# Kernel tuning notes

Measured on AMD Instinct MI355X. Metric: run time of the kernel, lower is better.

Reference implementation:

```python
import jax, jax.numpy as jnp
import numpy as np

B, S, N, E = 4, 256, 257, 256  # batch, seq_len, num_nodes (=S+1), num_edges (=S)
IN, OUT, EDIM = 128, 128, 16


def setup_inputs() -> dict:
    key = jax.random.key(0)
    k = jax.random.split(key, 7)
    x = jax.random.normal(k[0], (B, S, N, IN), jnp.float32)
    ei = jax.random.randint(k[1], (B, S, E, 2), 0, N)
    drop = jax.random.uniform(k[2], (B, S, E, 2)) < 0.05
    edge_index = jnp.where(drop, -1, ei)
    edge_attr = jax.random.normal(k[3], (B, S, E, EDIM), jnp.float32)
    node_mask = jnp.ones((B, S, N), dtype=bool)  # accepted but unused by forward
    edge_mask = jax.random.uniform(k[4], (B, S, E)) > 0.1
    W = jax.random.normal(k[5], (IN, OUT), jnp.float32) * (1.0 / np.sqrt(IN))
    a = jax.random.normal(k[6], (2 * OUT + EDIM, 1), jnp.float32) * 0.05
    return {"x": x, "edge_index": edge_index, "edge_attr": edge_attr,
            "node_mask": node_mask, "edge_mask": edge_mask, "W": W, "a": a}


def reference(x, edge_index, edge_attr, node_mask, edge_mask, W, a):
    # x: [B,S,N,IN] -> h: [B,S,N,D]
    h = x @ W
    Bq, Sq = h.shape[0], h.shape[1]
    src_idx = edge_index[..., 0]  # [B,S,E]
    tgt_idx = edge_index[..., 1]

    def gather(idx):  # [B,S,E] -> [B,S,E,D], gather node features along node dim
        return jnp.take_along_axis(h, jnp.clip(idx, 0, None)[..., None], axis=2)

    # src/tgt features, zeroed where index < 0 (invalid edge endpoint)
    src = jnp.where((src_idx >= 0)[..., None], gather(src_idx), 0.0)
    tgt = jnp.where((tgt_idx >= 0)[..., None], gather(tgt_idx), 0.0)

    # attention logits over concatenated [src | tgt | edge_attr]
    cat = jnp.concatenate([src, tgt, edge_attr], axis=-1)  # [B,S,E,2D+edim]
    e = jax.nn.leaky_relu((cat @ a)[..., 0], negative_slope=0.2)  # [B,S,E]
    e = jnp.where(edge_mask, e, -jnp.inf)
    # rows with no finite entry are zeroed (-> uniform softmax), as in torch code
    all_invalid = ~jnp.isfinite(e).any(axis=-1, keepdims=True)
    e = jnp.where(all_invalid, 0.0, e)
    alpha = jax.nn.softmax(e, axis=-1)  # [B,S,E]

    # masked edges get index 0 (they still contribute alpha-weighted feats to node 0,
    # matching the original scatter semantics)
    vsrc = jnp.where(edge_mask, src_idx, 0)
    vtgt = jnp.where(edge_mask, tgt_idx, 0)
    x_src = jnp.take_along_axis(h, vsrc[..., None], axis=2) * alpha[..., None]
    x_tgt = jnp.take_along_axis(h, vtgt[..., None], axis=2) * alpha[..., None]

    # scatter-add over edges into node buffer (equivalent to the torch 5D
    # scatter_ + sum over the edge dim, without materializing [B,S,E,N,D])
    bi = jnp.arange(Bq)[:, None, None]
    si = jnp.arange(Sq)[None, :, None]
    agg = (jnp.zeros(h.shape, h.dtype)
           .at[bi, si, vtgt].add(x_src)
           .at[bi, si, vsrc].add(x_tgt))
    return jax.nn.elu(agg)
```

## Files before the change

kernel.cpp:

```cpp
#include <hip/hip_runtime.h>
#include <cfloat>
#include <cmath>


#define BB 4
#define SS 256
#define NNODE 257
#define EE 256
#define DIN 128
#define DOUT 128
#define EDIMC 16
#define NMASK (BB * SS * EE)
#define MROWS (BB * SS * NNODE)

#define WS_FLAG_OFF  0
#define WS_MASK_OFF  1024
#define WS_ALPHA_OFF 266240
#define WS_PQ_OFF    (WS_ALPHA_OFF + NMASK * 4)
#define WS_PT_OFF    (WS_PQ_OFF + MROWS * 4)
#define WS_NEEDED    (WS_PT_OFF + MROWS * 4)

__global__ void detect_mask_kernel(const unsigned int* __restrict__ m, int* flag) {
    unsigned int v = 0;
    for (int i = threadIdx.x; i < 256; i += 64) v |= m[i];
    int bad = (v > 1u) ? 1 : 0;
    bad = __any(bad) ? 1 : 0;
    if (threadIdx.x == 0) *flag = bad;
}

__global__ __launch_bounds__(256) void mask_canon_kernel(
        const int* __restrict__ m32, const unsigned char* __restrict__ m8,
        const int* __restrict__ flag, unsigned char* __restrict__ out) {
    const bool byteLayout = (*flag != 0);
    int i = blockIdx.x * 256 + threadIdx.x;
    if (i < NMASK) out[i] = byteLayout ? (m8[i] != 0) : (m32[i] != 0);
}

__global__ __launch_bounds__(256) void gemm_kernel(const float* __restrict__ x,
                                                   const float* __restrict__ W,
                                                   const float* __restrict__ a,
                                                   float* __restrict__ h,
                                                   float* __restrict__ pq,
                                                   float* __restrict__ pt) {
    __shared__ float xs[32][132];
    __shared__ float wsh[32][132];
    const int tid = threadIdx.x;
    const long m0 = (long)blockIdx.x * 128;
    const int tm = tid >> 4;
    const int tn = tid & 15;
    const int mr = tm * 8, nr = tn * 8;
    float acc[8][8];
#pragma unroll
    for (int i = 0; i < 8; ++i)
#pragma unroll
        for (int j = 0; j < 8; ++j) acc[i][j] = 0.f;

    for (int kt = 0; kt < 4; ++kt) {
#pragma unroll
        for (int j = 0; j < 4; ++j) {
            int idx = j * 256 + tid;
            int row = idx >> 3;
            int kq  = idx & 7;
            float4 v = *reinterpret_cast<const float4*>(
                x + (m0 + row) * DIN + kt * 32 + kq * 4);
            xs[kq * 4 + 0][row] = v.x;
            xs[kq * 4 + 1][row] = v.y;
            xs[kq * 4 + 2][row] = v.z;
            xs[kq * 4 + 3][row] = v.w;
        }
#pragma unroll
        for (int j = 0; j < 4; ++j) {
            int idx = j * 256 + tid;
            int row = idx >> 5;
            int nq  = idx & 31;
            float4 v = *reinterpret_cast<const float4*>(
                W + (kt * 32 + row) * DOUT + nq * 4);
            *reinterpret_cast<float4*>(&wsh[row][nq * 4]) = v;
        }
        __syncthreads();
#pragma unroll
        for (int k = 0; k < 32; ++k) {
            float4 a0 = *reinterpret_cast<const float4*>(&xs[k][mr]);
            float4 a1 = *reinterpret_cast<const float4*>(&xs[k][mr + 4]);
            float4 b0 = *reinterpret_cast<const float4*>(&wsh[k][nr]);
            float4 b1 = *reinterpret_cast<const float4*>(&wsh[k][nr + 4]);
            float av[8] = {a0.x, a0.y, a0.z, a0.w, a1.x, a1.y, a1.z, a1.w};
            float bv[8] = {b0.x, b0.y, b0.z, b0.w, b1.x, b1.y, b1.z, b1.w};
#pragma unroll
            for (int i = 0; i < 8; ++i)
#pragma unroll
                for (int jj = 0; jj < 8; ++jj)
                    acc[i][jj] = fmaf(av[i], bv[jj], acc[i][jj]);
        }
        __syncthreads();
    }
#pragma unroll
    for (int i = 0; i < 8; ++i) {
        float* dst = h + (m0 + mr + i) * DOUT + nr;
        *reinterpret_cast<float4*>(dst) =
            make_float4(acc[i][0], acc[i][1], acc[i][2], acc[i][3]);
        *reinterpret_cast<float4*>(dst + 4) =
            make_float4(acc[i][4], acc[i][5], acc[i][6], acc[i][7]);
    }

    if (pq != nullptr) {
        float aq[8], at_[8];
#pragma unroll
        for (int j = 0; j < 8; ++j) {
            aq[j]  = a[nr + j];
            at_[j] = a[DOUT + nr + j];
        }
#pragma unroll
        for (int i = 0; i < 8; ++i) {
            float s = 0.f, t = 0.f;
#pragma unroll
            for (int j = 0; j < 8; ++j) {
                s = fmaf(acc[i][j], aq[j], s);
                t = fmaf(acc[i][j], at_[j], t);
            }
#pragma unroll
            for (int o = 1; o < 16; o <<= 1) {
                s += __shfl_xor(s, o);
                t += __shfl_xor(t, o);
            }
            if (tn == 0) {
                pq[m0 + mr + i] = s;
                pt[m0 + mr + i] = t;
            }
        }
    }
}

__global__ __launch_bounds__(256) void alpha2_kernel(
        const float* __restrict__ pq, const float* __restrict__ pt,
        const int* __restrict__ eidx, const float* __restrict__ eattr,
        const unsigned char* __restrict__ emask, const float* __restrict__ a,
        float* __restrict__ alpha_out) {
    __shared__ float ae[EDIMC];
    __shared__ float red[4];
    __shared__ int redi[4];
    const int tid = threadIdx.x;
    const int bs = blockIdx.x;
    const int lane = tid & 63, wave = tid >> 6;
    if (tid < EDIMC) ae[tid] = a[2 * DOUT + tid];
    __syncthreads();

    const long ebase = (long)bs * EE + tid;
    const int si = eidx[2 * ebase];
    const int ti = eidx[2 * ebase + 1];
    const float4* ea4 = reinterpret_cast<const float4*>(eattr + ebase * EDIMC);
    float dea = 0.f;
#pragma unroll
    for (int j = 0; j < 4; ++j) {
        float4 u = ea4[j];
        dea += u.x * ae[4 * j] + u.y * ae[4 * j + 1] +
               u.z * ae[4 * j + 2] + u.w * ae[4 * j + 3];
    }
    const long nb = (long)bs * NNODE;
    float val = (si >= 0 ? pq[nb + si] : 0.f) + (ti >= 0 ? pt[nb + ti] : 0.f) + dea;
    val = val > 0.f ? val : 0.2f * val;
    const bool m = emask[ebase] != 0;

    float lg = m ? val : -FLT_MAX;
    float wm = lg;
    int anyv = m ? 1 : 0;
#pragma unroll
    for (int o = 32; o > 0; o >>= 1) {
        wm = fmaxf(wm, __shfl_xor(wm, o));
        anyv |= __shfl_xor(anyv, o);
    }
    if (lane == 0) { red[wave] = wm; redi[wave] = anyv; }
    __syncthreads();
    const float gmax = fmaxf(fmaxf(red[0], red[1]), fmaxf(red[2], red[3]));
    const int ganyv = redi[0] | redi[1] | redi[2] | redi[3];
    float ex = m ? expf(val - gmax) : 0.f;
    float sm = ex;
#pragma unroll
    for (int o = 32; o > 0; o >>= 1) sm += __shfl_xor(sm, o);
    __syncthreads();
    if (lane == 0) red[wave] = sm;
    __syncthreads();
    const float gsum = red[0] + red[1] + red[2] + red[3];
    alpha_out[ebase] = ganyv ? ex / gsum : (1.0f / EE);
}

__global__ __launch_bounds__(256) void alpha_kernel(
        const float* __restrict__ h, const int* __restrict__ eidx,
        const float* __restrict__ eattr, const unsigned char* __restrict__ emask,
        const float* __restrict__ a, float* __restrict__ alpha_out) {
    __shared__ float pq[NNODE], pt[NNODE];
    __shared__ float ae[EDIMC];
    __shared__ float red[4];
    __shared__ int redi[4];
    const int tid = threadIdx.x;
    const int bs = blockIdx.x;
    const int lane = tid & 63, wave = tid >> 6;
    if (tid < EDIMC) ae[tid] = a[2 * DOUT + tid];
    const float a0 = a[lane], a1 = a[lane + 64];
    const float a2 = a[128 + lane], a3 = a[192 + lane];
    const float* hb = h + (long)bs * NNODE * DIN;
    for (int n = wave; n < NNODE; n += 4) {
        const float* hr = hb + n * DIN;
        float v0 = hr[lane], v1 = hr[lane + 64];
        float s = v0 * a0 + v1 * a1;
        float t = v0 * a2 + v1 * a3;
#pragma unroll
        for (int o = 32; o > 0; o >>= 1) {
            s += __shfl_xor(s, o);
            t += __shfl_xor(t, o);
        }
        if (lane == 0) { pq[n] = s; pt[n] = t; }
    }
    __syncthreads();

    const long ebase = (long)bs * EE + tid;
    const int si = eidx[2 * ebase];
    const int ti = eidx[2 * ebase + 1];
    const float4* ea4 = reinterpret_cast<const float4*>(eattr + ebase * EDIMC);
    float dea = 0.f;
#pragma unroll
    for (int j = 0; j < 4; ++j) {
        float4 u = ea4[j];
        dea += u.x * ae[4 * j] + u.y * ae[4 * j + 1] +
               u.z * ae[4 * j + 2] + u.w * ae[4 * j + 3];
    }
    float val = (si >= 0 ? pq[si] : 0.f) + (ti >= 0 ? pt[ti] : 0.f) + dea;
    val = val > 0.f ? val : 0.2f * val;
    const bool m = emask[ebase] != 0;

    float lg = m ? val : -FLT_MAX;
    float wm = lg;
    int anyv = m ? 1 : 0;
#pragma unroll
    for (int o = 32; o > 0; o >>= 1) {
        wm = fmaxf(wm, __shfl_xor(wm, o));
        anyv |= __shfl_xor(anyv, o);
    }
    if (lane == 0) { red[wave] = wm; redi[wave] = anyv; }
    __syncthreads();
    const float gmax = fmaxf(fmaxf(red[0], red[1]), fmaxf(red[2], red[3]));
    const int ganyv = redi[0] | redi[1] | redi[2] | redi[3];
    float ex = m ? expf(val - gmax) : 0.f;
    float sm = ex;
#pragma unroll
    for (int o = 32; o > 0; o >>= 1) sm += __shfl_xor(sm, o);
    __syncthreads();
    if (lane == 0) red[wave] = sm;
    __syncthreads();
    const float gsum = red[0] + red[1] + red[2] + red[3];
    alpha_out[ebase] = ganyv ? ex / gsum : (1.0f / EE);
}

#define DSL 16
#define PAD 17
__global__ __launch_bounds__(256) void agg_kernel(
        const float* __restrict__ h, const int* __restrict__ eidx,
        const unsigned char* __restrict__ emask, const float* __restrict__ alpha,
        float* __restrict__ out) {
    __shared__ float hs[NNODE * PAD];
    __shared__ float acc[NNODE * PAD];
    __shared__ float meta_a[EE];
    __shared__ int   meta_v[EE];
    const int tid = threadIdx.x;
    const int bs = blockIdx.x;
    const int dbase = blockIdx.y * DSL;
    const int slot = tid >> 4, d = tid & 15;

    const float* hb = h + (long)bs * NNODE * DIN + dbase;

    for (int i = tid; i < NNODE * 4; i += 256) {
        int row = i >> 2, q = i & 3;
        float4 v = *reinterpret_cast<const float4*>(hb + (long)row * DIN + q * 4);
        float* dst = &hs[row * PAD + q * 4];
        dst[0] = v.x; dst[1] = v.y; dst[2] = v.z; dst[3] = v.w;
    }
    for (int i = tid; i < NNODE * PAD; i += 256) acc[i] = 0.f;
    {
        const long eb = (long)bs * EE + tid;
        const int si = eidx[2 * eb];
        const int ti = eidx[2 * eb + 1];
        const bool m = emask[eb] != 0;
        int vs = m ? si : 0; if (vs < 0) vs += NNODE;
        int vt = m ? ti : 0; if (vt < 0) vt += NNODE;
        meta_a[tid] = alpha[eb];
        meta_v[tid] = vs | (vt << 16);
    }
    __syncthreads();

#pragma unroll 4
    for (int e0 = 0; e0 < EE; e0 += 16) {
        const int e = e0 + slot;
        const float al = meta_a[e];
        if (al != 0.f) {
            const int pv = meta_v[e];
            const int vs = pv & 0xffff, vt = pv >> 16;
            const float hsv = hs[vs * PAD + d];
            const float htv = hs[vt * PAD + d];
            atomicAdd(&acc[vt * PAD + d], al * hsv);
            atomicAdd(&acc[vs * PAD + d], al * htv);
        }
    }
    __syncthreads();

    float* ob = out + (long)bs * NNODE * DIN + dbase;
    for (int n = slot; n < NNODE; n += 16) {
        const float v = acc[n * PAD + d];
        ob[(long)n * DIN + d] = v > 0.f ? v : expm1f(v);
    }
}

extern "C" void kernel_launch(void* const* d_in, const int* in_sizes, int n_in,
                              void* d_out, int out_size, void* d_ws, size_t ws_size,
                              hipStream_t stream) {
    const float* x     = (const float*)d_in[0];
    const int* eidx    = (const int*)d_in[1];
    const float* eattr = (const float*)d_in[2];
    const void* emraw  = d_in[4];
    const float* W     = (const float*)d_in[5];
    const float* a     = (const float*)d_in[6];
    float* out = (float*)d_out;

    char* ws = (char*)d_ws;
    int* flag            = (int*)(ws + WS_FLAG_OFF);
    unsigned char* mask8 = (unsigned char*)(ws + WS_MASK_OFF);
    float* alpha         = (float*)(ws + WS_ALPHA_OFF);
    float* h             = out;
    const bool fused     = (ws_size >= (size_t)WS_NEEDED);
    float* pq            = fused ? (float*)(ws + WS_PQ_OFF) : nullptr;
    float* pt            = fused ? (float*)(ws + WS_PT_OFF) : nullptr;

    detect_mask_kernel<<<1, 64, 0, stream>>>((const unsigned int*)emraw, flag);
    mask_canon_kernel<<<NMASK / 256, 256, 0, stream>>>(
        (const int*)emraw, (const unsigned char*)emraw, flag, mask8);

    const int M_BLOCKS = MROWS / 128;
    gemm_kernel<<<M_BLOCKS, 256, 0, stream>>>(x, W, a, h, pq, pt);
    if (fused) {
        alpha2_kernel<<<BB * SS, 256, 0, stream>>>(pq, pt, eidx, eattr, mask8, a, alpha);
    } else {
        alpha_kernel<<<BB * SS, 256, 0, stream>>>(h, eidx, eattr, mask8, a, alpha);
    }
    agg_kernel<<<dim3(BB * SS, 8), 256, 0, stream>>>(h, eidx, mask8, alpha, out);
}
```

Baseline: 626.9 us.

## Use split-bf16 MFMA GEMM for projection and widen aggregation blocks

Replaces the FP32 SIMT GEMM with a matrix-core kernel that splits x and W into high and low bf16 parts and accumulates three MFMA products, which keeps close to FP32 accuracy. A small prep kernel writes W transposed as bf16 hi/lo into the workspace. The attention projections pq/pt are now reduced through shared-memory atomics. Separately, the aggregation kernel moves to 512 threads so 32 edges are processed per iteration. The GEMM rewrite targets compute time in the large projection, at the cost of three MFMAs per tile, extra conversion work, and a larger workspace requirement.

```diff
diff --git a/kernel.cpp b/kernel.cpp
--- a/kernel.cpp
+++ b/kernel.cpp
@@ -18,7 +18,21 @@
 #define WS_ALPHA_OFF 266240
 #define WS_PQ_OFF    (WS_ALPHA_OFF + NMASK * 4)
 #define WS_PT_OFF    (WS_PQ_OFF + MROWS * 4)
-#define WS_NEEDED    (WS_PT_OFF + MROWS * 4)
+#define WS_WTHI_OFF  (WS_PT_OFF + MROWS * 4)
+#define WS_WTLO_OFF  (WS_WTHI_OFF + DIN * DOUT * 2)
+#define WS_NEEDED    (WS_WTLO_OFF + DIN * DOUT * 2)
+
+typedef __attribute__((ext_vector_type(8))) short bf16x8;
+typedef __attribute__((ext_vector_type(4))) float f32x4;
+
+__device__ __forceinline__ unsigned short f2bf(float f) {
+    unsigned u = __float_as_uint(f);
+    u += 0x7fff + ((u >> 16) & 1);
+    return (unsigned short)(u >> 16);
+}
+__device__ __forceinline__ float bf2f(unsigned short h) {
+    return __uint_as_float((unsigned)h << 16);
+}
 
 __global__ void detect_mask_kernel(const unsigned int* __restrict__ m, int* flag) {
     unsigned int v = 0;
@@ -36,43 +50,185 @@
     if (i < NMASK) out[i] = byteLayout ? (m8[i] != 0) : (m32[i] != 0);
 }
 
+__global__ __launch_bounds__(256) void wprep_kernel(
+        const float* __restrict__ W, unsigned short* __restrict__ wthi,
+        unsigned short* __restrict__ wtlo) {
+    const int tid = threadIdx.x;
+    for (int i = tid; i < DIN * DOUT; i += 256) {
+        const int k = i >> 7, n = i & 127;
+        const float w = W[i];
+        const unsigned short hi = f2bf(w);
+        const unsigned short lo = f2bf(w - bf2f(hi));
+        wthi[n * DIN + k] = hi;
+        wtlo[n * DIN + k] = lo;
+    }
+}
+
+#define XPAD 40
+__global__ __launch_bounds__(256) void mfma_gemm_kernel(
+        const float* __restrict__ x, const unsigned short* __restrict__ wthi,
+        const unsigned short* __restrict__ wtlo, const float* __restrict__ a,
+        float* __restrict__ h, float* __restrict__ pq, float* __restrict__ pt) {
+    __shared__ unsigned short xhi[128][XPAD];
+    __shared__ unsigned short xlo[128][XPAD];
+    __shared__ unsigned short bhi[128][XPAD];
+    __shared__ unsigned short blo[128][XPAD];
+    __shared__ float pqs[128], pts[128];
+
+    const int tid = threadIdx.x;
+    const long m0 = (long)blockIdx.x * 128;
+    const int wave = tid >> 6, lane = tid & 63;
+    const int wm = wave >> 1, wn = wave & 1;
+    const int lrow = lane & 15;
+    const int lk8 = (lane >> 4) * 8;
+
+    if (tid < 128) { pqs[tid] = 0.f; pts[tid] = 0.f; }
+
+    f32x4 acc[4][4];
+#pragma unroll
+    for (int i = 0; i < 4; ++i)
+#pragma unroll
+        for (int j = 0; j < 4; ++j) acc[i][j] = (f32x4){0.f, 0.f, 0.f, 0.f};
+
+    const int srow = tid >> 1;
+    const int sk = (tid & 1) * 16;
+
+    for (int kt = 0; kt < 4; ++kt) {
+        __syncthreads();
+        {
+            const float* src = x + (m0 + srow) * DIN + kt * 32 + sk;
+#pragma unroll
+            for (int q = 0; q < 4; ++q) {
+                float4 v = *reinterpret_cast<const float4*>(src + q * 4);
+                ushort4 hi, lo;
+                hi.x = f2bf(v.x); lo.x = f2bf(v.x - bf2f(hi.x));
+                hi.y = f2bf(v.y); lo.y = f2bf(v.y - bf2f(hi.y));
+                hi.z = f2bf(v.z); lo.z = f2bf(v.z - bf2f(hi.z));
+                hi.w = f2bf(v.w); lo.w = f2bf(v.w - bf2f(hi.w));
+                *reinterpret_cast<ushort4*>(&xhi[srow][sk + q * 4]) = hi;
+                *reinterpret_cast<ushort4*>(&xlo[srow][sk + q * 4]) = lo;
+            }
+        }
+        {
+            const int n = tid >> 1;
+            const int kh = (tid & 1) * 16;
+            const unsigned short* sh = wthi + n * DIN + kt * 32 + kh;
+            const unsigned short* sl = wtlo + n * DIN + kt * 32 + kh;
+            *reinterpret_cast<uint4*>(&bhi[n][kh]) =
+                *reinterpret_cast<const uint4*>(sh);
+            *reinterpret_cast<uint4*>(&bhi[n][kh + 8]) =
+                *reinterpret_cast<const uint4*>(sh + 8);
+            *reinterpret_cast<uint4*>(&blo[n][kh]) =
+                *reinterpret_cast<const uint4*>(sl);
+            *reinterpret_cast<uint4*>(&blo[n][kh + 8]) =
+                *reinterpret_cast<const uint4*>(sl + 8);
+        }
+        __syncthreads();
+
+        bf16x8 Bh[4], Bl[4];
+#pragma unroll
+        for (int fn = 0; fn < 4; ++fn) {
+            const int n = wn * 64 + fn * 16 + lrow;
+            Bh[fn] = *reinterpret_cast<const bf16x8*>(&bhi[n][lk8]);
+            Bl[fn] = *reinterpret_cast<const bf16x8*>(&blo[n][lk8]);
+        }
+#pragma unroll
+        for (int fm = 0; fm < 4; ++fm) {
+            const int r = wm * 64 + fm * 16 + lrow;
+            bf16x8 Ah = *reinterpret_cast<const bf16x8*>(&xhi[r][lk8]);
+            bf16x8 Al = *reinterpret_cast<const bf16x8*>(&xlo[r][lk8]);
+#pragma unroll
+            for (int fn = 0; fn < 4; ++fn)
+                acc[fm][fn] = __builtin_amdgcn_mfma_f32_16x16x32_bf16(
+                    Ah, Bh[fn], acc[fm][fn], 0, 0, 0);
+#pragma unroll
+            for (int fn = 0; fn < 4; ++fn)
+                acc[fm][fn] = __builtin_amdgcn_mfma_f32_16x16x32_bf16(
+                    Ah, Bl[fn], acc[fm][fn], 0, 0, 0);
+#pragma unroll
+            for (int fn = 0; fn < 4; ++fn)
+                acc[fm][fn] = __builtin_amdgcn_mfma_f32_16x16x32_bf16(
+                    Al, Bh[fn], acc[fm][fn], 0, 0, 0);
+        }
+    }
+
+    const int qrow = (lane >> 4) * 4;
+    const int ccol = lane & 15;
+#pragma unroll
+    for (int fm = 0; fm < 4; ++fm) {
+#pragma unroll
+        for (int fn = 0; fn < 4; ++fn) {
+            float* dst = h + (m0 + wm * 64 + fm * 16 + qrow) * DOUT +
+                         wn * 64 + fn * 16 + ccol;
+#pragma unroll
+            for (int r = 0; r < 4; ++r) dst[(long)r * DOUT] = acc[fm][fn][r];
+        }
+    }
+
+    if (pq != nullptr) {
+        float aq[4], at_[4];
+#pragma unroll
+        for (int fn = 0; fn < 4; ++fn) {
+            aq[fn]  = a[wn * 64 + fn * 16 + ccol];
+            at_[fn] = a[DOUT + wn * 64 + fn * 16 + ccol];
+        }
+#pragma unroll
+        for (int fm = 0; fm < 4; ++fm) {
+#pragma unroll
+            for (int r = 0; r < 4; ++r) {
+                float s = 0.f, t = 0.f;
+#pragma unroll
+                for (int fn = 0; fn < 4; ++fn) {
+                    s = fmaf(acc[fm][fn][r], aq[fn], s);
+                    t = fmaf(acc[fm][fn][r], at_[fn], t);
+                }
+#pragma unroll
+                for (int o = 1; o < 16; o <<= 1) {
+                    s += __shfl_xor(s, o);
+                    t += __shfl_xor(t, o);
+                }
+                if (ccol == 0) {
+                    atomicAdd(&pqs[wm * 64 + fm * 16 + qrow + r], s);
+                    atomicAdd(&pts[wm * 64 + fm * 16 + qrow + r], t);
+                }
+            }
+        }
+        __syncthreads();
+        if (tid < 128) {
+            pq[m0 + tid] = pqs[tid];
+            pt[m0 + tid] = pts[tid];
+        }
+    }
+}
+
 __global__ __launch_bounds__(256) void gemm_kernel(const float* __restrict__ x,
                                                    const float* __restrict__ W,
-                                                   const float* __restrict__ a,
-                                                   float* __restrict__ h,
-                                                   float* __restrict__ pq,
-                                                   float* __restrict__ pt) {
+                                                   float* __restrict__ h) {
     __shared__ float xs[32][132];
     __shared__ float wsh[32][132];
     const int tid = threadIdx.x;
     const long m0 = (long)blockIdx.x * 128;
-    const int tm = tid >> 4;
-    const int tn = tid & 15;
+    const int tm = tid >> 4, tn = tid & 15;
     const int mr = tm * 8, nr = tn * 8;
     float acc[8][8];
 #pragma unroll
     for (int i = 0; i < 8; ++i)
 #pragma unroll
         for (int j = 0; j < 8; ++j) acc[i][j] = 0.f;
-
     for (int kt = 0; kt < 4; ++kt) {
 #pragma unroll
         for (int j = 0; j < 4; ++j) {
             int idx = j * 256 + tid;
-            int row = idx >> 3;
-            int kq  = idx & 7;
+            int row = idx >> 3, kq = idx & 7;
             float4 v = *reinterpret_cast<const float4*>(
                 x + (m0 + row) * DIN + kt * 32 + kq * 4);
-            xs[kq * 4 + 0][row] = v.x;
-            xs[kq * 4 + 1][row] = v.y;
-            xs[kq * 4 + 2][row] = v.z;
-            xs[kq * 4 + 3][row] = v.w;
+            xs[kq * 4 + 0][row] = v.x; xs[kq * 4 + 1][row] = v.y;
+            xs[kq * 4 + 2][row] = v.z; xs[kq * 4 + 3][row] = v.w;
         }
 #pragma unroll
         for (int j = 0; j < 4; ++j) {
             int idx = j * 256 + tid;
-            int row = idx >> 5;
-            int nq  = idx & 31;
+            int row = idx >> 5, nq = idx & 31;
             float4 v = *reinterpret_cast<const float4*>(
                 W + (kt * 32 + row) * DOUT + nq * 4);
             *reinterpret_cast<float4*>(&wsh[row][nq * 4]) = v;
@@ -101,33 +257,6 @@
             make_float4(acc[i][0], acc[i][1], acc[i][2], acc[i][3]);
         *reinterpret_cast<float4*>(dst + 4) =
             make_float4(acc[i][4], acc[i][5], acc[i][6], acc[i][7]);
-    }
-
-    if (pq != nullptr) {
-        float aq[8], at_[8];
-#pragma unroll
-        for (int j = 0; j < 8; ++j) {
-            aq[j]  = a[nr + j];
-            at_[j] = a[DOUT + nr + j];
-        }
-#pragma unroll
-        for (int i = 0; i < 8; ++i) {
-            float s = 0.f, t = 0.f;
-#pragma unroll
-            for (int j = 0; j < 8; ++j) {
-                s = fmaf(acc[i][j], aq[j], s);
-                t = fmaf(acc[i][j], at_[j], t);
-            }
-#pragma unroll
-            for (int o = 1; o < 16; o <<= 1) {
-                s += __shfl_xor(s, o);
-                t += __shfl_xor(t, o);
-            }
-            if (tn == 0) {
-                pq[m0 + mr + i] = s;
-                pt[m0 + mr + i] = t;
-            }
-        }
     }
 }
 
@@ -161,8 +290,7 @@
     val = val > 0.f ? val : 0.2f * val;
     const bool m = emask[ebase] != 0;
 
-    float lg = m ? val : -FLT_MAX;
-    float wm = lg;
+    float wm = m ? val : -FLT_MAX;
     int anyv = m ? 1 : 0;
 #pragma unroll
     for (int o = 32; o > 0; o >>= 1) {
@@ -228,8 +356,7 @@
     val = val > 0.f ? val : 0.2f * val;
     const bool m = emask[ebase] != 0;
 
-    float lg = m ? val : -FLT_MAX;
-    float wm = lg;
+    float wm = m ? val : -FLT_MAX;
     int anyv = m ? 1 : 0;
 #pragma unroll
     for (int o = 32; o > 0; o >>= 1) {
@@ -253,7 +380,7 @@
 
 #define DSL 16
 #define PAD 17
-__global__ __launch_bounds__(256) void agg_kernel(
+__global__ __launch_bounds__(512) void agg_kernel(
         const float* __restrict__ h, const int* __restrict__ eidx,
         const unsigned char* __restrict__ emask, const float* __restrict__ alpha,
         float* __restrict__ out) {
@@ -268,14 +395,14 @@
 
     const float* hb = h + (long)bs * NNODE * DIN + dbase;
 
-    for (int i = tid; i < NNODE * 4; i += 256) {
+    for (int i = tid; i < NNODE * 4; i += 512) {
         int row = i >> 2, q = i & 3;
         float4 v = *reinterpret_cast<const float4*>(hb + (long)row * DIN + q * 4);
         float* dst = &hs[row * PAD + q * 4];
         dst[0] = v.x; dst[1] = v.y; dst[2] = v.z; dst[3] = v.w;
     }
-    for (int i = tid; i < NNODE * PAD; i += 256) acc[i] = 0.f;
-    {
+    for (int i = tid; i < NNODE * PAD; i += 512) acc[i] = 0.f;
+    if (tid < EE) {
         const long eb = (long)bs * EE + tid;
         const int si = eidx[2 * eb];
         const int ti = eidx[2 * eb + 1];
@@ -288,7 +415,7 @@
     __syncthreads();
 
 #pragma unroll 4
-    for (int e0 = 0; e0 < EE; e0 += 16) {
+    for (int e0 = 0; e0 < EE; e0 += 32) {
         const int e = e0 + slot;
         const float al = meta_a[e];
         if (al != 0.f) {
@@ -303,7 +430,7 @@
     __syncthreads();
 
     float* ob = out + (long)bs * NNODE * DIN + dbase;
-    for (int n = slot; n < NNODE; n += 16) {
+    for (int n = slot; n < NNODE; n += 32) {
         const float v = acc[n * PAD + d];
         ob[(long)n * DIN + d] = v > 0.f ? v : expm1f(v);
     }
@@ -328,17 +455,21 @@
     const bool fused     = (ws_size >= (size_t)WS_NEEDED);
     float* pq            = fused ? (float*)(ws + WS_PQ_OFF) : nullptr;
     float* pt            = fused ? (float*)(ws + WS_PT_OFF) : nullptr;
+    unsigned short* wthi = (unsigned short*)(ws + WS_WTHI_OFF);
+    unsigned short* wtlo = (unsigned short*)(ws + WS_WTLO_OFF);
 
     detect_mask_kernel<<<1, 64, 0, stream>>>((const unsigned int*)emraw, flag);
     mask_canon_kernel<<<NMASK / 256, 256, 0, stream>>>(
         (const int*)emraw, (const unsigned char*)emraw, flag, mask8);
 
     const int M_BLOCKS = MROWS / 128;
-    gemm_kernel<<<M_BLOCKS, 256, 0, stream>>>(x, W, a, h, pq, pt);
     if (fused) {
+        wprep_kernel<<<1, 256, 0, stream>>>(W, wthi, wtlo);
+        mfma_gemm_kernel<<<M_BLOCKS, 256, 0, stream>>>(x, wthi, wtlo, a, h, pq, pt);
         alpha2_kernel<<<BB * SS, 256, 0, stream>>>(pq, pt, eidx, eattr, mask8, a, alpha);
     } else {
+        gemm_kernel<<<M_BLOCKS, 256, 0, stream>>>(x, W, h);
         alpha_kernel<<<BB * SS, 256, 0, stream>>>(h, eidx, eattr, mask8, a, alpha);
     }
-    agg_kernel<<<dim3(BB * SS, 8), 256, 0, stream>>>(h, eidx, mask8, alpha, out);
-}
+    agg_kernel<<<dim3(BB * SS, 8), 512, 0, stream>>>(h, eidx, mask8, alpha, out);
+}
```

Result: slower. 642.6 us (+2.5%).

## Fuse projection, attention and aggregation per graph using linearity of W

Applied to the files above, without the earlier changes.

Because the scatter-add is linear, the kernel aggregates raw x rows weighted by alpha first and multiplies by W afterwards, all in one per-(b,s) block. Attention logits come from x·(W a) vectors precomputed in a tiny prep kernel, so the full h matrix is never materialised. The final 257x128x128 product uses bf16 MFMA with hi/lo splitting (three products) to keep near-fp32 accuracy. This removes the large h write and reread and two kernel launches. In exchange it adds shared-memory atomics on a large LDS buffer, which limits occupancy, and a small accuracy change from the split-bf16 arithmetic.

```diff
diff --git a/kernel.cpp b/kernel.cpp
--- a/kernel.cpp
+++ b/kernel.cpp
@@ -15,10 +15,24 @@
 
 #define WS_FLAG_OFF  0
 #define WS_MASK_OFF  1024
-#define WS_ALPHA_OFF 266240
-#define WS_PQ_OFF    (WS_ALPHA_OFF + NMASK * 4)
-#define WS_PT_OFF    (WS_PQ_OFF + MROWS * 4)
-#define WS_NEEDED    (WS_PT_OFF + MROWS * 4)
+#define WS_WTHI_OFF  266240
+#define WS_WTLO_OFF  (WS_WTHI_OFF + 32768)
+#define WS_WAQ_OFF   (WS_WTLO_OFF + 32768)
+#define WS_WAT_OFF   (WS_WAQ_OFF + 512)
+#define WS_ALPHA_OFF (WS_WAT_OFF + 512)
+#define WS_NEEDED    (WS_ALPHA_OFF + NMASK * 4)
+
+typedef __attribute__((ext_vector_type(8))) short bf16x8;
+typedef __attribute__((ext_vector_type(4))) float f32x4;
+
+__device__ __forceinline__ unsigned short f2bf(float f) {
+    unsigned u = __float_as_uint(f);
+    u += 0x7fff + ((u >> 16) & 1);
+    return (unsigned short)(u >> 16);
+}
+__device__ __forceinline__ float bf2f(unsigned short h) {
+    return __uint_as_float((unsigned)h << 16);
+}
 
 __global__ void detect_mask_kernel(const unsigned int* __restrict__ m, int* flag) {
     unsigned int v = 0;
@@ -36,43 +50,249 @@
     if (i < NMASK) out[i] = byteLayout ? (m8[i] != 0) : (m32[i] != 0);
 }
 
+__global__ __launch_bounds__(256) void wprep_kernel(
+        const float* __restrict__ W, const float* __restrict__ a,
+        unsigned short* __restrict__ wthi, unsigned short* __restrict__ wtlo,
+        float* __restrict__ waq, float* __restrict__ wat) {
+    const int tid = threadIdx.x;
+    for (int i = tid; i < DIN * DOUT; i += 256) {
+        const int k = i >> 7, n = i & 127;
+        const float w = W[i];
+        const unsigned short hi = f2bf(w);
+        const unsigned short lo = f2bf(w - bf2f(hi));
+        wthi[n * DIN + k] = hi;
+        wtlo[n * DIN + k] = lo;
+    }
+    if (tid < DIN) {
+        const float* wr = W + tid * DOUT;
+        float sq = 0.f, st = 0.f;
+        for (int n = 0; n < DOUT; n += 4) {
+            float4 w4 = *reinterpret_cast<const float4*>(wr + n);
+            float4 aq = *reinterpret_cast<const float4*>(a + n);
+            float4 at4 = *reinterpret_cast<const float4*>(a + DOUT + n);
+            sq += w4.x * aq.x + w4.y * aq.y + w4.z * aq.z + w4.w * aq.w;
+            st += w4.x * at4.x + w4.y * at4.y + w4.z * at4.z + w4.w * at4.w;
+        }
+        waq[tid] = sq;
+        wat[tid] = st;
+    }
+}
+
+#define PADR 130
+#define WTP  132
+__global__ __launch_bounds__(512) void fused_kernel(
+        const float* __restrict__ x, const int* __restrict__ eidx,
+        const float* __restrict__ eattr, const unsigned char* __restrict__ emask,
+        const float* __restrict__ a,
+        const unsigned short* __restrict__ wthi,
+        const unsigned short* __restrict__ wtlo,
+        const float* __restrict__ waq, const float* __restrict__ wat,
+        float* __restrict__ out) {
+    __shared__ float aggx[272 * PADR];
+    __shared__ __align__(16) char ubuf[2 * 32 * WTP * 2];
+    float* pq    = (float*)ubuf;
+    float* pt    = pq + NNODE;
+    float* alpha = pt + NNODE;
+    int*   meta  = (int*)(alpha + EE);
+    float* red   = (float*)(meta + EE);
+    int*   redi  = (int*)(red + 8);
+    unsigned short* wtile = (unsigned short*)ubuf;
+
+    const int tid = threadIdx.x;
+    const int lane = tid & 63, wv = tid >> 6;
+    const int bs = blockIdx.x;
+    const float* xp = x + (long)bs * NNODE * DIN;
+
+    for (int i = tid; i < 272 * PADR; i += 512) aggx[i] = 0.f;
+
+    {
+        const float wq0 = waq[lane], wq1 = waq[lane + 64];
+        const float wt0 = wat[lane], wt1 = wat[lane + 64];
+        for (int n = wv; n < NNODE; n += 8) {
+            const float x0 = xp[n * DIN + lane];
+            const float x1 = xp[n * DIN + lane + 64];
+            float s = fmaf(x0, wq0, x1 * wq1);
+            float t = fmaf(x0, wt0, x1 * wt1);
+#pragma unroll
+            for (int o = 32; o > 0; o >>= 1) {
+                s += __shfl_xor(s, o);
+                t += __shfl_xor(t, o);
+            }
+            if (lane == 0) { pq[n] = s; pt[n] = t; }
+        }
+    }
+    __syncthreads();
+
+    float val = 0.f; bool m = false;
+    if (tid < EE) {
+        const long eb = (long)bs * EE + tid;
+        const int si = eidx[2 * eb];
+        const int ti = eidx[2 * eb + 1];
+        const float4* ea4 = reinterpret_cast<const float4*>(eattr + eb * EDIMC);
+        float dea = 0.f;
+#pragma unroll
+        for (int j = 0; j < 4; ++j) {
+            float4 u = ea4[j];
+            const float4 av = *reinterpret_cast<const float4*>(a + 2 * DOUT + 4 * j);
+            dea += u.x * av.x + u.y * av.y + u.z * av.z + u.w * av.w;
+        }
+        val = (si >= 0 ? pq[si] : 0.f) + (ti >= 0 ? pt[ti] : 0.f) + dea;
+        val = val > 0.f ? val : 0.2f * val;
+        m = emask[eb] != 0;
+        int vs = m ? si : 0; if (vs < 0) vs += NNODE;
+        int vt = m ? ti : 0; if (vt < 0) vt += NNODE;
+        meta[tid] = vs | (vt << 16);
+
+        float wm = m ? val : -FLT_MAX;
+        int anyv = m ? 1 : 0;
+#pragma unroll
+        for (int o = 32; o > 0; o >>= 1) {
+            wm = fmaxf(wm, __shfl_xor(wm, o));
+            anyv |= __shfl_xor(anyv, o);
+        }
+        if (lane == 0) { red[wv] = wm; redi[wv] = anyv; }
+    }
+    __syncthreads();
+    if (tid < EE) {
+        const float gmax = fmaxf(fmaxf(red[0], red[1]), fmaxf(red[2], red[3]));
+        const int ganyv = redi[0] | redi[1] | redi[2] | redi[3];
+        float ex = m ? expf(val - gmax) : 0.f;
+        float sm = ex;
+#pragma unroll
+        for (int o = 32; o > 0; o >>= 1) sm += __shfl_xor(sm, o);
+        __syncthreads();
+        if (lane == 0) red[wv] = sm;
+        __syncthreads();
+        const float gsum = red[0] + red[1] + red[2] + red[3];
+        alpha[tid] = ganyv ? ex / gsum : (1.0f / EE);
+    } else {
+        __syncthreads();
+        __syncthreads();
+    }
+    __syncthreads();
+
+    {
+        const int eslot = tid >> 4;
+        const int d0 = (tid & 15) * 8;
+        for (int e0 = 0; e0 < EE; e0 += 32) {
+            const int e = e0 + eslot;
+            const float al = alpha[e];
+            if (al != 0.f) {
+                const int pv = meta[e];
+                const int vs = pv & 0xffff, vt = pv >> 16;
+                const float* xs_ = xp + (long)vs * DIN + d0;
+                const float* xt_ = xp + (long)vt * DIN + d0;
+                const float4 s0 = *reinterpret_cast<const float4*>(xs_);
+                const float4 s1 = *reinterpret_cast<const float4*>(xs_ + 4);
+                const float4 t0 = *reinterpret_cast<const float4*>(xt_);
+                const float4 t1 = *reinterpret_cast<const float4*>(xt_ + 4);
+                float* rt_ = &aggx[vt * PADR + d0];
+                float* rs_ = &aggx[vs * PADR + d0];
+                atomicAdd(rt_ + 0, al * s0.x); atomicAdd(rt_ + 1, al * s0.y);
+                atomicAdd(rt_ + 2, al * s0.z); atomicAdd(rt_ + 3, al * s0.w);
+                atomicAdd(rt_ + 4, al * s1.x); atomicAdd(rt_ + 5, al * s1.y);
+                atomicAdd(rt_ + 6, al * s1.z); atomicAdd(rt_ + 7, al * s1.w);
+                atomicAdd(rs_ + 0, al * t0.x); atomicAdd(rs_ + 1, al * t0.y);
+                atomicAdd(rs_ + 2, al * t0.z); atomicAdd(rs_ + 3, al * t0.w);
+                atomicAdd(rs_ + 4, al * t1.x); atomicAdd(rs_ + 5, al * t1.y);
+                atomicAdd(rs_ + 6, al * t1.z); atomicAdd(rs_ + 7, al * t1.w);
+            }
+        }
+    }
+
+    const int lrow = lane & 15;
+    const int lk8 = (lane >> 4) * 8;
+    const int qrow = (lane >> 4) * 4;
+    float* ob = out + (long)bs * NNODE * DIN;
+    for (int nc = 0; nc < 4; ++nc) {
+        __syncthreads();
+        {
+            const int nl = tid >> 4, k8 = (tid & 15) * 8;
+            const int gn = nc * 32 + nl;
+            *reinterpret_cast<uint4*>(&wtile[nl * WTP + k8]) =
+                *reinterpret_cast<const uint4*>(&wthi[gn * DIN + k8]);
+            *reinterpret_cast<uint4*>(&wtile[32 * WTP + nl * WTP + k8]) =
+                *reinterpret_cast<const uint4*>(&wtlo[gn * DIN + k8]);
+        }
+        __syncthreads();
+        for (int rt = wv; rt < 17; rt += 8) {
+            f32x4 acc0 = {0.f, 0.f, 0.f, 0.f};
+            f32x4 acc1 = {0.f, 0.f, 0.f, 0.f};
+#pragma unroll
+            for (int kt = 0; kt < 4; ++kt) {
+                const float* ap = &aggx[(rt * 16 + lrow) * PADR + kt * 32 + lk8];
+                float av[8];
+                *reinterpret_cast<float4*>(&av[0]) =
+                    *reinterpret_cast<const float4*>(ap);
+                *reinterpret_cast<float4*>(&av[4]) =
+                    *reinterpret_cast<const float4*>(ap + 4);
+                bf16x8 Ah, Al;
+#pragma unroll
+                for (int j = 0; j < 8; ++j) {
+                    const unsigned short hi = f2bf(av[j]);
+                    Ah[j] = (short)hi;
+                    Al[j] = (short)f2bf(av[j] - bf2f(hi));
+                }
+                const int bo = kt * 32 + lk8;
+                bf16x8 Bh0 = *reinterpret_cast<const bf16x8*>(
+                    &wtile[lrow * WTP + bo]);
+                bf16x8 Bl0 = *reinterpret_cast<const bf16x8*>(
+                    &wtile[32 * WTP + lrow * WTP + bo]);
+                bf16x8 Bh1 = *reinterpret_cast<const bf16x8*>(
+                    &wtile[(16 + lrow) * WTP + bo]);
+                bf16x8 Bl1 = *reinterpret_cast<const bf16x8*>(
+                    &wtile[32 * WTP + (16 + lrow) * WTP + bo]);
+                acc0 = __builtin_amdgcn_mfma_f32_16x16x32_bf16(Ah, Bh0, acc0, 0, 0, 0);
+                acc0 = __builtin_amdgcn_mfma_f32_16x16x32_bf16(Ah, Bl0, acc0, 0, 0, 0);
+                acc0 = __builtin_amdgcn_mfma_f32_16x16x32_bf16(Al, Bh0, acc0, 0, 0, 0);
+                acc1 = __builtin_amdgcn_mfma_f32_16x16x32_bf16(Ah, Bh1, acc1, 0, 0, 0);
+                acc1 = __builtin_amdgcn_mfma_f32_16x16x32_bf16(Ah, Bl1, acc1, 0, 0, 0);
+                acc1 = __builtin_amdgcn_mfma_f32_16x16x32_bf16(Al, Bh1, acc1, 0, 0, 0);
+            }
+#pragma unroll
+            for (int r = 0; r < 4; ++r) {
+                const int row = rt * 16 + qrow + r;
+                if (row < NNODE) {
+                    float v0 = acc0[r];
+                    v0 = v0 > 0.f ? v0 : expm1f(v0);
+                    ob[(long)row * DIN + nc * 32 + lrow] = v0;
+                    float v1 = acc1[r];
+                    v1 = v1 > 0.f ? v1 : expm1f(v1);
+                    ob[(long)row * DIN + nc * 32 + 16 + lrow] = v1;
+                }
+            }
+        }
+    }
+}
+
 __global__ __launch_bounds__(256) void gemm_kernel(const float* __restrict__ x,
                                                    const float* __restrict__ W,
-                                                   const float* __restrict__ a,
-                                                   float* __restrict__ h,
-                                                   float* __restrict__ pq,
-                                                   float* __restrict__ pt) {
+                                                   float* __restrict__ h) {
     __shared__ float xs[32][132];
     __shared__ float wsh[32][132];
     const int tid = threadIdx.x;
     const long m0 = (long)blockIdx.x * 128;
-    const int tm = tid >> 4;
-    const int tn = tid & 15;
+    const int tm = tid >> 4, tn = tid & 15;
     const int mr = tm * 8, nr = tn * 8;
     float acc[8][8];
 #pragma unroll
     for (int i = 0; i < 8; ++i)
 #pragma unroll
         for (int j = 0; j < 8; ++j) acc[i][j] = 0.f;
-
     for (int kt = 0; kt < 4; ++kt) {
 #pragma unroll
         for (int j = 0; j < 4; ++j) {
             int idx = j * 256 + tid;
-            int row = idx >> 3;
-            int kq  = idx & 7;
+            int row = idx >> 3, kq = idx & 7;
             float4 v = *reinterpret_cast<const float4*>(
                 x + (m0 + row) * DIN + kt * 32 + kq * 4);
-            xs[kq * 4 + 0][row] = v.x;
-            xs[kq * 4 + 1][row] = v.y;
-            xs[kq * 4 + 2][row] = v.z;
-            xs[kq * 4 + 3][row] = v.w;
+            xs[kq * 4 + 0][row] = v.x; xs[kq * 4 + 1][row] = v.y;
+            xs[kq * 4 + 2][row] = v.z; xs[kq * 4 + 3][row] = v.w;
         }
 #pragma unroll
         for (int j = 0; j < 4; ++j) {
             int idx = j * 256 + tid;
-            int row = idx >> 5;
-            int nq  = idx & 31;
+            int row = idx >> 5, nq = idx & 31;
             float4 v = *reinterpret_cast<const float4*>(
                 W + (kt * 32 + row) * DOUT + nq * 4);
             *reinterpret_cast<float4*>(&wsh[row][nq * 4]) = v;
@@ -102,86 +322,6 @@
         *reinterpret_cast<float4*>(dst + 4) =
             make_float4(acc[i][4], acc[i][5], acc[i][6], acc[i][7]);
     }
-
-    if (pq != nullptr) {
-        float aq[8], at_[8];
-#pragma unroll
-        for (int j = 0; j < 8; ++j) {
-            aq[j]  = a[nr + j];
-            at_[j] = a[DOUT + nr + j];
-        }
-#pragma unroll
-        for (int i = 0; i < 8; ++i) {
-            float s = 0.f, t = 0.f;
-#pragma unroll
-            for (int j = 0; j < 8; ++j) {
-                s = fmaf(acc[i][j], aq[j], s);
-                t = fmaf(acc[i][j], at_[j], t);
-            }
-#pragma unroll
-            for (int o = 1; o < 16; o <<= 1) {
-                s += __shfl_xor(s, o);
-                t += __shfl_xor(t, o);
-            }
-            if (tn == 0) {
-                pq[m0 + mr + i] = s;
-                pt[m0 + mr + i] = t;
-            }
-        }
-    }
-}
-
-__global__ __launch_bounds__(256) void alpha2_kernel(
-        const float* __restrict__ pq, const float* __restrict__ pt,
-        const int* __restrict__ eidx, const float* __restrict__ eattr,
-        const unsigned char* __restrict__ emask, const float* __restrict__ a,
-        float* __restrict__ alpha_out) {
-    __shared__ float ae[EDIMC];
-    __shared__ float red[4];
-    __shared__ int redi[4];
-    const int tid = threadIdx.x;
-    const int bs = blockIdx.x;
-    const int lane = tid & 63, wave = tid >> 6;
-    if (tid < EDIMC) ae[tid] = a[2 * DOUT + tid];
-    __syncthreads();
-
-    const long ebase = (long)bs * EE + tid;
-    const int si = eidx[2 * ebase];
-    const int ti = eidx[2 * ebase + 1];
-    const float4* ea4 = reinterpret_cast<const float4*>(eattr + ebase * EDIMC);
-    float dea = 0.f;
-#pragma unroll
-    for (int j = 0; j < 4; ++j) {
-        float4 u = ea4[j];
-        dea += u.x * ae[4 * j] + u.y * ae[4 * j + 1] +
-               u.z * ae[4 * j + 2] + u.w * ae[4 * j + 3];
-    }
-    const long nb = (long)bs * NNODE;
-    float val = (si >= 0 ? pq[nb + si] : 0.f) + (ti >= 0 ? pt[nb + ti] : 0.f) + dea;
-    val = val > 0.f ? val : 0.2f * val;
-    const bool m = emask[ebase] != 0;
-
-    float lg = m ? val : -FLT_MAX;
-    float wm = lg;
-    int anyv = m ? 1 : 0;
-#pragma unroll
-    for (int o = 32; o > 0; o >>= 1) {
-        wm = fmaxf(wm, __shfl_xor(wm, o));
-        anyv |= __shfl_xor(anyv, o);
-    }
-    if (lane == 0) { red[wave] = wm; redi[wave] = anyv; }
-    __syncthreads();
-    const float gmax = fmaxf(fmaxf(red[0], red[1]), fmaxf(red[2], red[3]));
-    const int ganyv = redi[0] | redi[1] | redi[2] | redi[3];
-    float ex = m ? expf(val - gmax) : 0.f;
-    float sm = ex;
-#pragma unroll
-    for (int o = 32; o > 0; o >>= 1) sm += __shfl_xor(sm, o);
-    __syncthreads();
-    if (lane == 0) red[wave] = sm;
-    __syncthreads();
-    const float gsum = red[0] + red[1] + red[2] + red[3];
-    alpha_out[ebase] = ganyv ? ex / gsum : (1.0f / EE);
 }
 
 __global__ __launch_bounds__(256) void alpha_kernel(
@@ -212,7 +352,6 @@
         if (lane == 0) { pq[n] = s; pt[n] = t; }
     }
     __syncthreads();
-
     const long ebase = (long)bs * EE + tid;
     const int si = eidx[2 * ebase];
     const int ti = eidx[2 * ebase + 1];
@@ -227,9 +366,7 @@
     float val = (si >= 0 ? pq[si] : 0.f) + (ti >= 0 ? pt[ti] : 0.f) + dea;
     val = val > 0.f ? val : 0.2f * val;
     const bool m = emask[ebase] != 0;
-
-    float lg = m ? val : -FLT_MAX;
-    float wm = lg;
+    float wm = m ? val : -FLT_MAX;
     int anyv = m ? 1 : 0;
 #pragma unroll
     for (int o = 32; o > 0; o >>= 1) {
@@ -253,7 +390,7 @@
 
 #define DSL 16
 #define PAD 17
-__global__ __launch_bounds__(256) void agg_kernel(
+__global__ __launch_bounds__(512) void agg_kernel(
         const float* __restrict__ h, const int* __restrict__ eidx,
         const unsigned char* __restrict__ emask, const float* __restrict__ alpha,
         float* __restrict__ out) {
@@ -265,17 +402,15 @@
     const int bs = blockIdx.x;
     const int dbase = blockIdx.y * DSL;
     const int slot = tid >> 4, d = tid & 15;
-
     const float* hb = h + (long)bs * NNODE * DIN + dbase;
-
-    for (int i = tid; i < NNODE * 4; i += 256) {
+    for (int i = tid; i < NNODE * 4; i += 512) {
         int row = i >> 2, q = i & 3;
         float4 v = *reinterpret_cast<const float4*>(hb + (long)row * DIN + q * 4);
         float* dst = &hs[row * PAD + q * 4];
         dst[0] = v.x; dst[1] = v.y; dst[2] = v.z; dst[3] = v.w;
     }
-    for (int i = tid; i < NNODE * PAD; i += 256) acc[i] = 0.f;
-    {
+    for (int i = tid; i < NNODE * PAD; i += 512) acc[i] = 0.f;
+    if (tid < EE) {
         const long eb = (long)bs * EE + tid;
         const int si = eidx[2 * eb];
         const int ti = eidx[2 * eb + 1];
@@ -286,9 +421,8 @@
         meta_v[tid] = vs | (vt << 16);
     }
     __syncthreads();
-
 #pragma unroll 4
-    for (int e0 = 0; e0 < EE; e0 += 16) {
+    for (int e0 = 0; e0 < EE; e0 += 32) {
         const int e = e0 + slot;
         const float al = meta_a[e];
         if (al != 0.f) {
@@ -301,9 +435,8 @@
         }
     }
     __syncthreads();
-
     float* ob = out + (long)bs * NNODE * DIN + dbase;
-    for (int n = slot; n < NNODE; n += 16) {
+    for (int n = slot; n < NNODE; n += 32) {
         const float v = acc[n * PAD + d];
         ob[(long)n * DIN + d] = v > 0.f ? v : expm1f(v);
     }
@@ -323,22 +456,24 @@
     char* ws = (char*)d_ws;
     int* flag            = (int*)(ws + WS_FLAG_OFF);
     unsigned char* mask8 = (unsigned char*)(ws + WS_MASK_OFF);
+    unsigned short* wthi = (unsigned short*)(ws + WS_WTHI_OFF);
+    unsigned short* wtlo = (unsigned short*)(ws + WS_WTLO_OFF);
+    float* waq           = (float*)(ws + WS_WAQ_OFF);
+    float* wat           = (float*)(ws + WS_WAT_OFF);
     float* alpha         = (float*)(ws + WS_ALPHA_OFF);
-    float* h             = out;
-    const bool fused     = (ws_size >= (size_t)WS_NEEDED);
-    float* pq            = fused ? (float*)(ws + WS_PQ_OFF) : nullptr;
-    float* pt            = fused ? (float*)(ws + WS_PT_OFF) : nullptr;
 
     detect_mask_kernel<<<1, 64, 0, stream>>>((const unsigned int*)emraw, flag);
     mask_canon_kernel<<<NMASK / 256, 256, 0, stream>>>(
         (const int*)emraw, (const unsigned char*)emraw, flag, mask8);
 
-    const int M_BLOCKS = MROWS / 128;
-    gemm_kernel<<<M_BLOCKS, 256, 0, stream>>>(x, W, a, h, pq, pt);
-    if (fused) {
-        alpha2_kernel<<<BB * SS, 256, 0, stream>>>(pq, pt, eidx, eattr, mask8, a, alpha);
+    if (ws_size >= (size_t)WS_NEEDED) {
+        wprep_kernel<<<1, 256, 0, stream>>>(W, a, wthi, wtlo, waq, wat);
+        fused_kernel<<<BB * SS, 512, 0, stream>>>(
+            x, eidx, eattr, mask8, a, wthi, wtlo, waq, wat, out);
     } else {
+        float* h = out;
+        gemm_kernel<<<MROWS / 128, 256, 0, stream>>>(x, W, h);
         alpha_kernel<<<BB * SS, 256, 0, stream>>>(h, eidx, eattr, mask8, a, alpha);
-    }
-    agg_kernel<<<dim3(BB * SS, 8), 256, 0, stream>>>(h, eidx, mask8, alpha, out);
-}
+        agg_kernel<<<dim3(BB * SS, 8), 512, 0, stream>>>(h, eidx, mask8, alpha, out);
+    }
+}
```

New measurement: 814.7 us. 1.3x slower.
